# Kernel tuning notes

Hardware: AMD Instinct MI355X
Metric: run time of the kernel (lower is better)

Reference implementation:

```python
import jax, jax.numpy as jnp
import numpy as np

Q = 4096  # num_quantizing
E = 256   # quantizing_dim


def setup_inputs() -> dict:
    key = jax.random.key(0)
    kx, kw = jax.random.split(key)
    x = jax.random.normal(kx, (16, 2048, E), dtype=jnp.float32)
    # nn.init.normal_(weight, mean=0.0, std=0.001)
    weight = 0.001 * jax.random.normal(kw, (Q, E), dtype=jnp.float32)
    return {"x": x, "weight": weight}


def reference(x, weight):
    # x: (*, E), weight: (Q, E)
    input_shape = x.shape
    xf = x.reshape(-1, weight.shape[1])  # (N, E)
    # Squared L2 distance via norm expansion (same argmin as sum(delta^2)):
    x2 = jnp.sum(xf * xf, axis=1, keepdims=True)          # (N, 1)
    w2 = jnp.sum(weight * weight, axis=1)                  # (Q,)
    dist = x2 - 2.0 * (xf @ weight.T) + w2                 # (N, Q)
    q_idx = jnp.argmin(dist, axis=1)                       # (N,)
    q_data = weight[q_idx]                                 # (N, E)
    return q_data.reshape(input_shape), q_idx.reshape(input_shape[:-1])
```

## Files before the change

### kernel.cpp

```cpp
#include <hip/hip_runtime.h>
#include <cfloat>
#include <climits>

constexpr int E  = 256;
constexpr int Qn = 4096;
constexpr float WSCALE = 4096.0f;


typedef _Float16 half8  __attribute__((ext_vector_type(8)));
typedef _Float16 half4v __attribute__((ext_vector_type(4)));
typedef float    f32x16 __attribute__((ext_vector_type(16)));

#define GAS __attribute__((address_space(1)))
#define LAS __attribute__((address_space(3)))

#define NEG_INF __int_as_float(0xFF800000)

__device__ inline bool lexlt(float a, int ai, float b, int bi) {
    return a < b || (a == b && ai < bi);
}

__global__ __launch_bounds__(256) void prep_kernel(
    const float* __restrict__ x, const float* __restrict__ w,
    _Float16* __restrict__ A16, _Float16* __restrict__ B16,
    float* __restrict__ x2, float* __restrict__ w2, int nxblocks)
{
    int blk  = blockIdx.x;
    int sub  = threadIdx.x >> 6;
    int lane = threadIdx.x & 63;
    bool isX = blk < nxblocks;
    int row  = (isX ? blk : blk - nxblocks) * 4 + sub;

    const float* src = isX ? x : w;
    float4 v = *(const float4*)(src + (size_t)row * E + lane * 4);

    float s = v.x * v.x + v.y * v.y + v.z * v.z + v.w * v.w;
    #pragma unroll
    for (int off = 32; off; off >>= 1) s += __shfl_xor(s, off);
    if (lane == 0) (isX ? x2 : w2)[row] = s;

    float sc = isX ? 1.0f : WSCALE;
    half4v h = { (_Float16)(v.x * sc), (_Float16)(v.y * sc),
                 (_Float16)(v.z * sc), (_Float16)(v.w * sc) };
    _Float16* dst16 = (isX ? A16 : B16) + (size_t)row * 256;
    *(half4v*)(dst16 + lane * 4) = h;
}

__device__ inline void ins4max(float K[4], float k) {
    #pragma unroll
    for (int t = 0; t < 4; ++t) {
        float mx = fmaxf(K[t], k);
        k = fminf(K[t], k);
        K[t] = mx;
    }
}

union SmemU {
    struct { _Float16 W[128 * 64]; _Float16 X[128 * 64]; } st;
    float2 mergeS[128 * 4];
};

__global__ __launch_bounds__(256, 4) void vq_mfma_kernel(
    const _Float16* __restrict__ A16,
    const _Float16* __restrict__ B16,
    float4* __restrict__ top4)
{
    __shared__ SmemU sm;

    const int tid  = threadIdx.x;
    const int w    = tid >> 6;
    const int lane = tid & 63;
    const int l31  = lane & 31;
    const int lh   = lane >> 5;
    const int rb   = blockIdx.x;
    const int cg   = blockIdx.y;

    const int wr = (w & 1) * 64;
    const int wc = (w >> 1) * 64;

    f32x16 acc[2][2];
    #pragma unroll
    for (int f = 0; f < 2; ++f)
        #pragma unroll
        for (int g = 0; g < 2; ++g)
            #pragma unroll
            for (int r = 0; r < 16; ++r) acc[f][g][r] = 0.0f;

    const _Float16* Ab16 = A16 + (size_t)rb * 128 * 256;
    const _Float16* Bb16 = B16 + (size_t)cg * 128 * 256;

    const int srow = lane >> 3;
    const int schk = lane & 7;

    for (int kt = 0; kt < 4; ++kt) {
        __syncthreads();
        #pragma unroll
        for (int inst = 0; inst < 4; ++inst) {
            int drow = w * 32 + inst * 8 + srow;
            int gchk = schk ^ (drow & 7);
            const _Float16* gW = Bb16 + (size_t)drow * 256 + kt * 64 + gchk * 8;
            const _Float16* gX = Ab16 + (size_t)drow * 256 + kt * 64 + gchk * 8;
            __builtin_amdgcn_global_load_lds((const GAS void*)gW,
                (LAS void*)(sm.st.W + w * 2048 + inst * 512), 16, 0, 0);
            __builtin_amdgcn_global_load_lds((const GAS void*)gX,
                (LAS void*)(sm.st.X + w * 2048 + inst * 512), 16, 0, 0);
        }
        __syncthreads();

        #pragma unroll
        for (int s = 0; s < 4; ++s) {
            const int kc = 2 * s + lh;
            half8 wf[2], xf[2];
            #pragma unroll
            for (int f = 0; f < 2; ++f) {
                int fr = wc + 32 * f + l31;
                wf[f] = *(const half8*)(sm.st.W + fr * 64 + ((kc ^ (fr & 7)) << 3));
                int xr = wr + 32 * f + l31;
                xf[f] = *(const half8*)(sm.st.X + xr * 64 + ((kc ^ (xr & 7)) << 3));
            }
            #pragma unroll
            for (int f = 0; f < 2; ++f)
                #pragma unroll
                for (int g = 0; g < 2; ++g)
                    acc[f][g] = __builtin_amdgcn_mfma_f32_32x32x16_f16(
                        wf[f], xf[g], acc[f][g], 0, 0, 0);
        }
    }

    float t1[2] = { NEG_INF, NEG_INF }, t2[2] = { NEG_INF, NEG_INF };

    #pragma unroll
    for (int f = 0; f < 2; ++f)
        #pragma unroll
        for (int r = 0; r < 16; ++r) {
            int m  = (r & 3) + 8 * (r >> 2) + 4 * lh;
            int qg = cg * 128 + wc + 32 * f + m;
            #pragma unroll
            for (int g = 0; g < 2; ++g) {
                float pk = __int_as_float(
                    (__float_as_int(acc[f][g][r]) & 0xFFFFF000) | qg);
                t2[g] = __builtin_amdgcn_fmed3f(t1[g], t2[g], pk);
                t1[g] = fmaxf(t1[g], pk);
            }
        }

    __syncthreads();

    #pragma unroll
    for (int g = 0; g < 2; ++g) {
        int rrow = wr + 32 * g + l31;
        sm.mergeS[rrow * 4 + ((w >> 1) * 2 + lh)] = make_float2(t1[g], t2[g]);
    }
    __syncthreads();

    if (tid < 128) {
        float K[4] = { NEG_INF, NEG_INF, NEG_INF, NEG_INF };
        #pragma unroll
        for (int sl = 0; sl < 4; ++sl) {
            float2 a = sm.mergeS[tid * 4 + sl];
            ins4max(K, a.x);
            ins4max(K, a.y);
        }
        top4[(size_t)(rb * 128 + tid) * 32 + cg] =
            make_float4(K[0], K[1], K[2], K[3]);
    }
}

__global__ __launch_bounds__(256) void finalize_kernel(
    const float4* __restrict__ top4, const float* __restrict__ x,
    const float* __restrict__ w, const float* __restrict__ x2,
    const float* __restrict__ w2, float* __restrict__ qdata,
    float* __restrict__ qidx)
{
    int row  = blockIdx.x * 4 + (threadIdx.x >> 6);
    int lane = threadIdx.x & 63;

    float cand[4];
    if (lane < 32) {
        float4 c4 = top4[(size_t)row * 32 + lane];
        cand[0] = c4.x; cand[1] = c4.y; cand[2] = c4.z; cand[3] = c4.w;
    } else {
        cand[0] = cand[1] = cand[2] = cand[3] = NEG_INF;
    }

    int chosen[4];
    #pragma unroll
    for (int p = 0; p < 4; ++p) {
        float cur = fmaxf(fmaxf(cand[0], cand[1]), fmaxf(cand[2], cand[3]));
        #pragma unroll
        for (int off = 32; off; off >>= 1)
            cur = fmaxf(cur, __shfl_xor(cur, off));
        int curb = __float_as_int(cur);
        chosen[p] = curb & 0xFFF;
        #pragma unroll
        for (int j = 0; j < 4; ++j)
            if (__float_as_int(cand[j]) == curb) cand[j] = NEG_INF;
    }

    float4 xv = *(const float4*)(x + (size_t)row * E + lane * 4);
    float d[4];
    #pragma unroll
    for (int j = 0; j < 4; ++j) {
        float4 wv = *(const float4*)(w + (size_t)chosen[j] * E + lane * 4);
        d[j] = xv.x * wv.x + xv.y * wv.y + xv.z * wv.z + xv.w * wv.w;
    }
    #pragma unroll
    for (int off = 32; off; off >>= 1) {
        #pragma unroll
        for (int j = 0; j < 4; ++j) d[j] += __shfl_xor(d[j], off);
    }

    float X2 = x2[row];
    float bs = FLT_MAX; int win = INT_MAX;
    #pragma unroll
    for (int j = 0; j < 4; ++j) {
        float s = (X2 - 2.0f * d[j]) + w2[chosen[j]];
        if (lexlt(s, chosen[j], bs, win)) { bs = s; win = chosen[j]; }
    }

    if (lane == 0) qidx[row] = (float)win;
    *(float4*)(qdata + (size_t)row * E + lane * 4) =
        *(const float4*)(w + (size_t)win * E + lane * 4);
}

constexpr int FBM = 64, FBN = 128, FBK = 64, FPAD = 4, FTH = 256;

__global__ __launch_bounds__(64) void row_sumsq_kernel(const float* __restrict__ src,
                                                       float* __restrict__ dst) {
    int row = blockIdx.x, lane = threadIdx.x;
    float4 v = ((const float4*)(src + (size_t)row * E))[lane];
    float s = v.x * v.x + v.y * v.y + v.z * v.z + v.w * v.w;
    #pragma unroll
    for (int off = 32; off > 0; off >>= 1) s += __shfl_down(s, off);
    if (lane == 0) dst[row] = s;
}

__global__ __launch_bounds__(FTH) void vq_fallback_kernel(
    const float* __restrict__ x, const float* __restrict__ w,
    const float* __restrict__ x2, const float* __restrict__ w2,
    float* __restrict__ qdata, float* __restrict__ qidx)
{
    __shared__ float xs[FBM][FBK + FPAD];
    __shared__ float ws[FBN][FBK + FPAD];
    __shared__ float redS[FBM][16];
    __shared__ int   redC[FBM][16];
    __shared__ int   bestC[FBM];

    const int tid = threadIdx.x, tr = tid >> 4, tc = tid & 15;
    const int r0 = blockIdx.x * FBM;
    float best[4]; int bidx[4];
    #pragma unroll
    for (int i = 0; i < 4; ++i) { best[i] = FLT_MAX; bidx[i] = 0x7FFFFFFF; }
    float x2r[4];
    #pragma unroll
    for (int i = 0; i < 4; ++i) x2r[i] = x2[r0 + tr + 16 * i];

    for (int qt = 0; qt < Qn / FBN; ++qt) {
        const int c0 = qt * FBN;
        float acc[4][8];
        #pragma unroll
        for (int i = 0; i < 4; ++i)
            #pragma unroll
            for (int j = 0; j < 8; ++j) acc[i][j] = 0.f;
        for (int kt = 0; kt < E / FBK; ++kt) {
            __syncthreads();
            const int kk = (tid & 15) * 4, rr = tid >> 4;
            #pragma unroll
            for (int m = 0; m < 4; ++m)
                *(float4*)&xs[m * 16 + rr][kk] =
                    *(const float4*)(x + (size_t)(r0 + m * 16 + rr) * E + kt * FBK + kk);
            #pragma unroll
            for (int m = 0; m < 8; ++m)
                *(float4*)&ws[m * 16 + rr][kk] =
                    *(const float4*)(w + (size_t)(c0 + m * 16 + rr) * E + kt * FBK + kk);
            __syncthreads();
            #pragma unroll
            for (int k4 = 0; k4 < FBK / 4; ++k4) {
                float4 a[4], bb[8];
                #pragma unroll
                for (int i = 0; i < 4; ++i) a[i] = *(const float4*)&xs[tr + 16 * i][k4 * 4];
                #pragma unroll
                for (int j = 0; j < 8; ++j) bb[j] = *(const float4*)&ws[tc + 16 * j][k4 * 4];
                #pragma unroll
                for (int i = 0; i < 4; ++i)
                    #pragma unroll
                    for (int j = 0; j < 8; ++j) {
                        acc[i][j] += a[i].x * bb[j].x; acc[i][j] += a[i].y * bb[j].y;
                        acc[i][j] += a[i].z * bb[j].z; acc[i][j] += a[i].w * bb[j].w;
                    }
            }
        }
        #pragma unroll
        for (int i = 0; i < 4; ++i)
            #pragma unroll
            for (int j = 0; j < 8; ++j) {
                int c = c0 + tc + 16 * j;
                float s = (x2r[i] - 2.0f * acc[i][j]) + w2[c];
                if (s < best[i]) { best[i] = s; bidx[i] = c; }
            }
    }
    #pragma unroll
    for (int i = 0; i < 4; ++i) { redS[tr + 16 * i][tc] = best[i]; redC[tr + 16 * i][tc] = bidx[i]; }
    __syncthreads();
    if (tid < FBM) {
        float bs = FLT_MAX; int bc = 0x7FFFFFFF;
        #pragma unroll
        for (int t = 0; t < 16; ++t) {
            float s = redS[tid][t]; int c = redC[tid][t];
            if (s < bs || (s == bs && c < bc)) { bs = s; bc = c; }
        }
        qidx[r0 + tid] = (float)bc; bestC[tid] = bc;
    }
    __syncthreads();
    for (int it = 0; it < FBM / 4; ++it) {
        int row = it * 4 + (tid >> 6), c = bestC[row], kk = (tid & 63) * 4;
        *(float4*)(qdata + (size_t)(r0 + row) * E + kk) = *(const float4*)(w + (size_t)c * E + kk);
    }
}

extern "C" void kernel_launch(void* const* d_in, const int* in_sizes, int n_in,
                              void* d_out, int out_size, void* d_ws, size_t ws_size,
                              hipStream_t stream) {
    const float* x = (const float*)d_in[0];
    const float* w = (const float*)d_in[1];
    const int N = in_sizes[0] / E;

    float* qdata = (float*)d_out;
    float* qidx  = (float*)d_out + (size_t)N * E;

    size_t off = 0;
    auto carve = [&](size_t bytes) { size_t p = off; off += (bytes + 255) & ~(size_t)255; return p; };
    size_t oA16 = carve((size_t)N  * 256 * sizeof(_Float16));
    size_t oB16 = carve((size_t)Qn * 256 * sizeof(_Float16));
    size_t ox2  = carve((size_t)N * sizeof(float));
    size_t ow2  = carve((size_t)Qn * sizeof(float));
    size_t oT   = carve((size_t)N * 32 * sizeof(float4));

    if (ws_size >= off && (N % 128) == 0) {
        char* ws = (char*)d_ws;
        _Float16* A16 = (_Float16*)(ws + oA16);
        _Float16* B16 = (_Float16*)(ws + oB16);
        float* x2    = (float*)(ws + ox2);
        float* w2    = (float*)(ws + ow2);
        float4* top4 = (float4*)(ws + oT);

        prep_kernel<<<N / 4 + Qn / 4, 256, 0, stream>>>(x, w, A16, B16, x2, w2, N / 4);
        vq_mfma_kernel<<<dim3(N / 128, Qn / 128), 256, 0, stream>>>(A16, B16, top4);
        finalize_kernel<<<N / 4, 256, 0, stream>>>(top4, x, w, x2, w2, qdata, qidx);
    } else {
        float* x2 = (float*)d_ws;
        float* w2 = x2 + N;
        row_sumsq_kernel<<<N, 64, 0, stream>>>(x, x2);
        row_sumsq_kernel<<<Qn, 64, 0, stream>>>(w, w2);
        vq_fallback_kernel<<<N / FBM, FTH, 0, stream>>>(x, w, x2, w2, qdata, qidx);
    }
}
```

Baseline: 201.6 us.

## Loop each block over eight codebook tiles and keep running top-3 per lane

Each MFMA block now walks eight 128-wide codebook column tiles in sequence instead of one, keeping a per-lane running top-3 of packed score/index values across tiles. Each block then writes one top-4 candidate set per row for its quarter of the codebook, shrinking the candidate buffer from 32 to 4 entries per row, and finalize merges them with a simple serial insert instead of wave-wide shuffle reductions. This cuts top-4 write and readback traffic and finalize work. In exchange the grid shrinks eightfold (256x4 blocks), X tiles are reloaded from global for each codebook tile, and merging fewer, coarser candidates changes which near-ties reach exact rescoring.

```diff
diff --git a/kernel.cpp b/kernel.cpp
--- a/kernel.cpp
+++ b/kernel.cpp
@@ -57,7 +57,7 @@
 
 union SmemU {
     struct { _Float16 W[128 * 64]; _Float16 X[128 * 64]; } st;
-    float2 mergeS[128 * 4];
+    float mS[128 * 12];
 };
 
 __global__ __launch_bounds__(256, 4) void vq_mfma_kernel(
@@ -73,95 +73,102 @@
     const int l31  = lane & 31;
     const int lh   = lane >> 5;
     const int rb   = blockIdx.x;
-    const int cg   = blockIdx.y;
+    const int qq   = blockIdx.y;
 
     const int wr = (w & 1) * 64;
     const int wc = (w >> 1) * 64;
 
-    f32x16 acc[2][2];
-    #pragma unroll
-    for (int f = 0; f < 2; ++f)
-        #pragma unroll
-        for (int g = 0; g < 2; ++g)
-            #pragma unroll
-            for (int r = 0; r < 16; ++r) acc[f][g][r] = 0.0f;
-
     const _Float16* Ab16 = A16 + (size_t)rb * 128 * 256;
-    const _Float16* Bb16 = B16 + (size_t)cg * 128 * 256;
 
     const int srow = lane >> 3;
     const int schk = lane & 7;
 
-    for (int kt = 0; kt < 4; ++kt) {
-        __syncthreads();
-        #pragma unroll
-        for (int inst = 0; inst < 4; ++inst) {
-            int drow = w * 32 + inst * 8 + srow;
-            int gchk = schk ^ (drow & 7);
-            const _Float16* gW = Bb16 + (size_t)drow * 256 + kt * 64 + gchk * 8;
-            const _Float16* gX = Ab16 + (size_t)drow * 256 + kt * 64 + gchk * 8;
-            __builtin_amdgcn_global_load_lds((const GAS void*)gW,
-                (LAS void*)(sm.st.W + w * 2048 + inst * 512), 16, 0, 0);
-            __builtin_amdgcn_global_load_lds((const GAS void*)gX,
-                (LAS void*)(sm.st.X + w * 2048 + inst * 512), 16, 0, 0);
+    float t1[2] = { NEG_INF, NEG_INF };
+    float t2[2] = { NEG_INF, NEG_INF };
+    float t3[2] = { NEG_INF, NEG_INF };
+
+    for (int cn = 0; cn < 8; ++cn) {
+        const int cg = qq * 8 + cn;
+        const _Float16* Bb16 = B16 + (size_t)cg * 128 * 256;
+
+        f32x16 acc[2][2];
+        #pragma unroll
+        for (int f = 0; f < 2; ++f)
+            #pragma unroll
+            for (int g = 0; g < 2; ++g)
+                #pragma unroll
+                for (int r = 0; r < 16; ++r) acc[f][g][r] = 0.0f;
+
+        for (int kt = 0; kt < 4; ++kt) {
+            __syncthreads();
+            #pragma unroll
+            for (int inst = 0; inst < 4; ++inst) {
+                int drow = w * 32 + inst * 8 + srow;
+                int gchk = schk ^ (drow & 7);
+                const _Float16* gW = Bb16 + (size_t)drow * 256 + kt * 64 + gchk * 8;
+                const _Float16* gX = Ab16 + (size_t)drow * 256 + kt * 64 + gchk * 8;
+                __builtin_amdgcn_global_load_lds((const GAS void*)gW,
+                    (LAS void*)(sm.st.W + w * 2048 + inst * 512), 16, 0, 0);
+                __builtin_amdgcn_global_load_lds((const GAS void*)gX,
+                    (LAS void*)(sm.st.X + w * 2048 + inst * 512), 16, 0, 0);
+            }
+            __syncthreads();
+
+            #pragma unroll
+            for (int s = 0; s < 4; ++s) {
+                const int kc = 2 * s + lh;
+                half8 wf[2], xf[2];
+                #pragma unroll
+                for (int f = 0; f < 2; ++f) {
+                    int fr = wc + 32 * f + l31;
+                    wf[f] = *(const half8*)(sm.st.W + fr * 64 + ((kc ^ (fr & 7)) << 3));
+                    int xr = wr + 32 * f + l31;
+                    xf[f] = *(const half8*)(sm.st.X + xr * 64 + ((kc ^ (xr & 7)) << 3));
+                }
+                #pragma unroll
+                for (int f = 0; f < 2; ++f)
+                    #pragma unroll
+                    for (int g = 0; g < 2; ++g)
+                        acc[f][g] = __builtin_amdgcn_mfma_f32_32x32x16_f16(
+                            wf[f], xf[g], acc[f][g], 0, 0, 0);
+            }
         }
-        __syncthreads();
-
-        #pragma unroll
-        for (int s = 0; s < 4; ++s) {
-            const int kc = 2 * s + lh;
-            half8 wf[2], xf[2];
-            #pragma unroll
-            for (int f = 0; f < 2; ++f) {
-                int fr = wc + 32 * f + l31;
-                wf[f] = *(const half8*)(sm.st.W + fr * 64 + ((kc ^ (fr & 7)) << 3));
-                int xr = wr + 32 * f + l31;
-                xf[f] = *(const half8*)(sm.st.X + xr * 64 + ((kc ^ (xr & 7)) << 3));
-            }
-            #pragma unroll
-            for (int f = 0; f < 2; ++f)
-                #pragma unroll
-                for (int g = 0; g < 2; ++g)
-                    acc[f][g] = __builtin_amdgcn_mfma_f32_32x32x16_f16(
-                        wf[f], xf[g], acc[f][g], 0, 0, 0);
-        }
-    }
-
-    float t1[2] = { NEG_INF, NEG_INF }, t2[2] = { NEG_INF, NEG_INF };
-
-    #pragma unroll
-    for (int f = 0; f < 2; ++f)
-        #pragma unroll
-        for (int r = 0; r < 16; ++r) {
-            int m  = (r & 3) + 8 * (r >> 2) + 4 * lh;
-            int qg = cg * 128 + wc + 32 * f + m;
-            #pragma unroll
-            for (int g = 0; g < 2; ++g) {
-                float pk = __int_as_float(
-                    (__float_as_int(acc[f][g][r]) & 0xFFFFF000) | qg);
-                t2[g] = __builtin_amdgcn_fmed3f(t1[g], t2[g], pk);
-                t1[g] = fmaxf(t1[g], pk);
-            }
-        }
+
+        #pragma unroll
+        for (int f = 0; f < 2; ++f)
+            #pragma unroll
+            for (int r = 0; r < 16; ++r) {
+                int m  = (r & 3) + 8 * (r >> 2) + 4 * lh;
+                int qg = cg * 128 + wc + 32 * f + m;
+                #pragma unroll
+                for (int g = 0; g < 2; ++g) {
+                    float pk = __int_as_float(
+                        (__float_as_int(acc[f][g][r]) & 0xFFFFF000) | qg);
+                    float mn = fminf(t2[g], pk);
+                    t3[g] = fmaxf(t3[g], mn);
+                    t2[g] = __builtin_amdgcn_fmed3f(t1[g], t2[g], pk);
+                    t1[g] = fmaxf(t1[g], pk);
+                }
+            }
+    }
 
     __syncthreads();
 
     #pragma unroll
     for (int g = 0; g < 2; ++g) {
         int rrow = wr + 32 * g + l31;
-        sm.mergeS[rrow * 4 + ((w >> 1) * 2 + lh)] = make_float2(t1[g], t2[g]);
+        int src  = (w >> 1) * 2 + lh;
+        sm.mS[rrow * 12 + src * 3 + 0] = t1[g];
+        sm.mS[rrow * 12 + src * 3 + 1] = t2[g];
+        sm.mS[rrow * 12 + src * 3 + 2] = t3[g];
     }
     __syncthreads();
 
     if (tid < 128) {
         float K[4] = { NEG_INF, NEG_INF, NEG_INF, NEG_INF };
         #pragma unroll
-        for (int sl = 0; sl < 4; ++sl) {
-            float2 a = sm.mergeS[tid * 4 + sl];
-            ins4max(K, a.x);
-            ins4max(K, a.y);
-        }
-        top4[(size_t)(rb * 128 + tid) * 32 + cg] =
+        for (int s = 0; s < 12; ++s) ins4max(K, sm.mS[tid * 12 + s]);
+        top4[(size_t)(rb * 128 + tid) * 4 + qq] =
             make_float4(K[0], K[1], K[2], K[3]);
     }
 }
@@ -175,27 +182,15 @@
     int row  = blockIdx.x * 4 + (threadIdx.x >> 6);
     int lane = threadIdx.x & 63;
 
-    float cand[4];
-    if (lane < 32) {
-        float4 c4 = top4[(size_t)row * 32 + lane];
-        cand[0] = c4.x; cand[1] = c4.y; cand[2] = c4.z; cand[3] = c4.w;
-    } else {
-        cand[0] = cand[1] = cand[2] = cand[3] = NEG_INF;
-    }
-
+    float K[4] = { NEG_INF, NEG_INF, NEG_INF, NEG_INF };
+    #pragma unroll
+    for (int j = 0; j < 4; ++j) {
+        float4 c = top4[(size_t)row * 4 + j];
+        ins4max(K, c.x); ins4max(K, c.y); ins4max(K, c.z); ins4max(K, c.w);
+    }
     int chosen[4];
     #pragma unroll
-    for (int p = 0; p < 4; ++p) {
-        float cur = fmaxf(fmaxf(cand[0], cand[1]), fmaxf(cand[2], cand[3]));
-        #pragma unroll
-        for (int off = 32; off; off >>= 1)
-            cur = fmaxf(cur, __shfl_xor(cur, off));
-        int curb = __float_as_int(cur);
-        chosen[p] = curb & 0xFFF;
-        #pragma unroll
-        for (int j = 0; j < 4; ++j)
-            if (__float_as_int(cand[j]) == curb) cand[j] = NEG_INF;
-    }
+    for (int j = 0; j < 4; ++j) chosen[j] = __float_as_int(K[j]) & 0xFFF;
 
     float4 xv = *(const float4*)(x + (size_t)row * E + lane * 4);
     float d[4];
@@ -334,7 +329,7 @@
     size_t oB16 = carve((size_t)Qn * 256 * sizeof(_Float16));
     size_t ox2  = carve((size_t)N * sizeof(float));
     size_t ow2  = carve((size_t)Qn * sizeof(float));
-    size_t oT   = carve((size_t)N * 32 * sizeof(float4));
+    size_t oT   = carve((size_t)N * 4 * sizeof(float4));
 
     if (ws_size >= off && (N % 128) == 0) {
         char* ws = (char*)d_ws;
@@ -345,7 +340,7 @@
         float4* top4 = (float4*)(ws + oT);
 
         prep_kernel<<<N / 4 + Qn / 4, 256, 0, stream>>>(x, w, A16, B16, x2, w2, N / 4);
-        vq_mfma_kernel<<<dim3(N / 128, Qn / 128), 256, 0, stream>>>(A16, B16, top4);
+        vq_mfma_kernel<<<dim3(N / 128, 4), 256, 0, stream>>>(A16, B16, top4);
         finalize_kernel<<<N / 4, 256, 0, stream>>>(top4, x, w, x2, w2, qdata, qidx);
     } else {
         float* x2 = (float*)d_ws;
```

Result: slower. 278.2 us (+38.0%).
